# Kernel optimization log

Hardware: AMD Instinct MI355X
Metric: run time of the kernel (lower is better)

The kernel has to match this reference:

```python
import jax, jax.numpy as jnp
import numpy as np

N_HEADS = 8

def gcn_conv(x, edge_index, W, b):
    # PyG GCNConv: add self-loops, symmetric normalization, linear transform + bias
    N = x.shape[0]
    loop = jnp.arange(N)
    src = jnp.concatenate([edge_index[0], loop])
    dst = jnp.concatenate([edge_index[1], loop])
    deg = jax.ops.segment_sum(jnp.ones(src.shape[0], dtype=x.dtype), dst, num_segments=N)
    dinv = jax.lax.rsqrt(jnp.maximum(deg, 1.0))  # deg >= 1 due to self-loops
    norm = dinv[src] * dinv[dst]                 # [E+N]
    h = x @ W                                    # [N, out]
    msg = h[src] * norm[:, None]                 # gather + scale
    return jax.ops.segment_sum(msg, dst, num_segments=N) + b

def layer_norm(x, g, b):
    mu = jnp.mean(x, axis=-1, keepdims=True)
    var = jnp.mean((x - mu) ** 2, axis=-1, keepdims=True)
    return (x - mu) * jax.lax.rsqrt(var + 1e-5) * g + b

def mha(q, kv, Wq, Wk, Wv, Wo):
    B, M, d = q.shape
    dh = d // N_HEADS
    Q = (q @ Wq).reshape(B, M, N_HEADS, dh)
    K = (kv @ Wk).reshape(B, kv.shape[1], N_HEADS, dh)
    V = (kv @ Wv).reshape(B, kv.shape[1], N_HEADS, dh)
    scale = jnp.asarray(1.0 / np.sqrt(dh), q.dtype)
    scores = jnp.einsum('bqhd,bkhd->bhqk', Q, K) * scale
    attn = jax.nn.softmax(scores, axis=-1)
    out = jnp.einsum('bhqk,bkhd->bqhd', attn, V).reshape(B, M, d)
    return out @ Wo

def setup_inputs() -> dict:
    key = jax.random.key(0)
    ks = jax.random.split(key, 24)
    B, M, d, dff, L = 32, 1024, 128, 512, 2
    N, E = B * M, 524288
    s = 0.02
    inp = {
        'enc_out_vari': jax.random.normal(ks[0], (B, M, d), jnp.float32),
        'x_enc': jax.random.normal(ks[1], (B, M, d), jnp.float32),
        'x_raw': jax.random.normal(ks[2], (N, d), jnp.float32),
        'edge_index': jax.random.randint(ks[3], (2, E), 0, N, jnp.int64 if jax.config.jax_enable_x64 else jnp.int32),
        'W_gcn1': s * jax.random.normal(ks[4], (d, d), jnp.float32),
        'b_gcn1': jnp.zeros((d,), jnp.float32),
        'W_gcn2': s * jax.random.normal(ks[5], (d, d), jnp.float32),
        'b_gcn2': jnp.zeros((d,), jnp.float32),
        'Wq': s * jax.random.normal(ks[6], (L, d, d), jnp.float32),
        'Wk': s * jax.random.normal(ks[7], (L, d, d), jnp.float32),
        'Wv': s * jax.random.normal(ks[8], (L, d, d), jnp.float32),
        'Wo': s * jax.random.normal(ks[9], (L, d, d), jnp.float32),
        'Wff1': s * jax.random.normal(ks[10], (L, d, dff), jnp.float32),
        'bff1': jnp.zeros((L, dff), jnp.float32),
        'Wff2': s * jax.random.normal(ks[11], (L, dff, d), jnp.float32),
        'bff2': jnp.zeros((L, d), jnp.float32),
        'ln1_g': jnp.ones((L, d), jnp.float32),
        'ln1_b': jnp.zeros((L, d), jnp.float32),
        'ln2_g': jnp.ones((L, d), jnp.float32),
        'ln2_b': jnp.zeros((L, d), jnp.float32),
    }
    return inp

def reference(enc_out_vari, x_enc, x_raw, edge_index, W_gcn1, b_gcn1, W_gcn2, b_gcn2,
              Wq, Wk, Wv, Wo, Wff1, bff1, Wff2, bff2, ln1_g, ln1_b, ln2_g, ln2_b):
    B, M, d = enc_out_vari.shape
    # GCN stack (dropout is identity in eval mode)
    x1 = jax.nn.relu(gcn_conv(x_raw, edge_index, W_gcn1, b_gcn1))
    x2 = jax.nn.relu(gcn_conv(x1, edge_index, W_gcn2, b_gcn2))
    x = x2.reshape(B, M, d)
    # Transformer encoder: cross-attention from enc_out_vari onto GCN features
    y = enc_out_vari
    L = Wq.shape[0]
    for l in range(L):
        a = mha(y, x, Wq[l], Wk[l], Wv[l], Wo[l])
        y = layer_norm(y + a, ln1_g[l], ln1_b[l])
        f = jax.nn.relu(y @ Wff1[l] + bff1[l]) @ Wff2[l] + bff2[l]
        y = layer_norm(y + f, ln2_g[l], ln2_b[l])
    return y
```

## Files before the change

### kernel.cpp

```cpp
#include <hip/hip_runtime.h>
#include <math.h>


typedef __attribute__((ext_vector_type(8)))  short short8;
typedef __attribute__((ext_vector_type(4)))  float f32x4;
typedef __attribute__((ext_vector_type(16))) float f32x16;

__device__ __forceinline__ unsigned short f2bf(float x) {
    unsigned u = __builtin_bit_cast(unsigned, x);
    u = (u + 0x7FFFu + ((u >> 16) & 1u)) >> 16;
    return (unsigned short)u;
}
__device__ __forceinline__ float bflo(unsigned u) { return __builtin_bit_cast(float, u << 16); }
__device__ __forceinline__ float bfhi(unsigned u) { return __builtin_bit_cast(float, u & 0xffff0000u); }
__device__ __forceinline__ float fast_exp2(float x) {
    float r; asm("v_exp_f32 %0, %1" : "=v"(r) : "v"(x)); return r;
}

__global__ void count_kernel(const int* __restrict__ dst, int* __restrict__ cnt, int E) {
    int e = blockIdx.x * 256 + threadIdx.x;
    if (e < E) atomicAdd(&cnt[dst[e]], 1);
}

__global__ __launch_bounds__(256)
void scanA_kernel(const int* __restrict__ cnt, int* __restrict__ partial)
{
    __shared__ int wsum[4];
    int t = threadIdx.x;
    int v = cnt[blockIdx.x * 256 + t];
    #pragma unroll
    for (int off = 32; off; off >>= 1) v += __shfl_xor(v, off, 64);
    if ((t & 63) == 0) wsum[t >> 6] = v;
    __syncthreads();
    if (t == 0) partial[blockIdx.x] = wsum[0] + wsum[1] + wsum[2] + wsum[3];
}

__global__ __launch_bounds__(128)
void scanB_kernel(const int* __restrict__ partial, int* __restrict__ base)
{
    __shared__ int p[128];
    int t = threadIdx.x;
    int v = partial[t];
    p[t] = v;
    __syncthreads();
    for (int o = 1; o < 128; o <<= 1) {
        int q = (t >= o) ? p[t - o] : 0;
        __syncthreads();
        p[t] += q;
        __syncthreads();
    }
    base[t] = p[t] - v;
}

__global__ __launch_bounds__(256)
void scanC_kernel(const int* __restrict__ cnt, const int* __restrict__ base,
                  int* __restrict__ off, int* __restrict__ cursor,
                  float* __restrict__ dinv, int N, int E)
{
    __shared__ int p[256];
    int t = threadIdx.x, b = blockIdx.x;
    int i = b * 256 + t;
    int c = cnt[i];
    p[t] = c;
    __syncthreads();
    for (int o = 1; o < 256; o <<= 1) {
        int q = (t >= o) ? p[t - o] : 0;
        __syncthreads();
        p[t] += q;
        __syncthreads();
    }
    int ex = base[b] + p[t] - c;
    off[i] = ex;
    cursor[i] = ex;
    dinv[i] = rsqrtf((float)c + 1.0f);
    if (b == 0 && t == 0) off[N] = E;
}

__global__ void place_kernel(const int* __restrict__ src, const int* __restrict__ dst,
                             int* __restrict__ cursor, int* __restrict__ csr_src, int E)
{
    int e = blockIdx.x * 256 + threadIdx.x;
    if (e < E) {
        int p = atomicAdd(&cursor[dst[e]], 1);
        csr_src[p] = src[e];
    }
}

__global__ void conv_kernel(const float* __restrict__ src, unsigned short* __restrict__ dst) {
    int i = blockIdx.x * 256 + threadIdx.x;
    float4 v = ((const float4*)src)[i];
    ushort4 h; h.x = f2bf(v.x); h.y = f2bf(v.y); h.z = f2bf(v.z); h.w = f2bf(v.w);
    ((ushort4*)dst)[i] = h;
}

__global__ void copyconv_kernel(const float* __restrict__ src, float* __restrict__ dstf,
                                unsigned short* __restrict__ dsth) {
    int i = blockIdx.x * 256 + threadIdx.x;
    float4 v = ((const float4*)src)[i];
    ((float4*)dstf)[i] = v;
    ushort4 h; h.x = f2bf(v.x); h.y = f2bf(v.y); h.z = f2bf(v.z); h.w = f2bf(v.w);
    ((ushort4*)dsth)[i] = h;
}

__global__ __launch_bounds__(256)
void wtrans_kernel(const float* Wg1, const float* Wg2, const float* Wq, const float* Wk,
                   const float* Wv, const float* Wo, const float* Wff1, const float* Wff2,
                   unsigned short* __restrict__ out)
{
    const int slot = blockIdx.y;
    const float* src; int ks; int Ns; size_t doff; float scale = 1.0f;
    if      (slot == 0)  { src = Wg1;                        ks = 7; Ns = 128; doff = 0; }
    else if (slot == 1)  { src = Wg2;                        ks = 7; Ns = 128; doff = 16384; }
    else if (slot <= 3)  { src = Wq  + (slot - 2)  * 16384;  ks = 7; Ns = 128; doff = 32768  + (size_t)(slot - 2)  * 16384; scale = 0.36067376022f; }
    else if (slot <= 5)  { src = Wk  + (slot - 4)  * 16384;  ks = 7; Ns = 128; doff = 65536  + (size_t)(slot - 4)  * 32768; }
    else if (slot <= 7)  { src = Wv  + (slot - 6)  * 16384;  ks = 7; Ns = 128; doff = 65536  + (size_t)(slot - 6)  * 32768 + 16384; }
    else if (slot <= 9)  { src = Wo  + (slot - 8)  * 16384;  ks = 7; Ns = 128; doff = 131072 + (size_t)(slot - 8)  * 16384; }
    else if (slot <= 11) { src = Wff1 + (slot - 10) * 65536; ks = 7; Ns = 512; doff = 163840 + (size_t)(slot - 10) * 65536; }
    else                 { src = Wff2 + (slot - 12) * 65536; ks = 9; Ns = 128; doff = 294912 + (size_t)(slot - 12) * 65536; }
    const int total = Ns << ks;
    int id = blockIdx.x * 256 + threadIdx.x;
    if (id >= total) return;
    int n = id >> ks;
    int k = id & ((1 << ks) - 1);
    out[doff + id] = f2bf(src[(size_t)k * Ns + n] * scale);
}

__global__ __launch_bounds__(256)
void gemm64_kernel(const unsigned short* __restrict__ A,
                   const unsigned short* __restrict__ Wt,
                   void* __restrict__ C, void* __restrict__ C2, int K,
                   const float* __restrict__ bias, const float* __restrict__ rowscale,
                   int relu, int mode)
{
    __shared__ unsigned short As[64 * 72];
    __shared__ unsigned short Ws[64 * 72];

    const int tid  = threadIdx.x;
    const int lane = tid & 63, wave = tid >> 6;
    const int m31 = lane & 31, hi = lane >> 5;
    const int row0 = blockIdx.x * 64;
    const int c0   = blockIdx.y * 64;
    const int wrow = (wave & 1) * 32;
    const int wcol = (wave >> 1) * 32;
    const int sr = tid >> 2, sk = (tid & 3) * 16;

    f32x16 acc = {};

    for (int kt = 0; kt < K; kt += 64) {
        if (kt) __syncthreads();
        *(short8*)&As[sr * 72 + sk]     = *(const short8*)&A [(size_t)(row0 + sr) * K + kt + sk];
        *(short8*)&As[sr * 72 + sk + 8] = *(const short8*)&A [(size_t)(row0 + sr) * K + kt + sk + 8];
        *(short8*)&Ws[sr * 72 + sk]     = *(const short8*)&Wt[(size_t)(c0   + sr) * K + kt + sk];
        *(short8*)&Ws[sr * 72 + sk + 8] = *(const short8*)&Wt[(size_t)(c0   + sr) * K + kt + sk + 8];
        __syncthreads();
        #pragma unroll
        for (int ks = 0; ks < 4; ++ks) {
            short8 af = *(const short8*)&As[(wrow + m31) * 72 + ks * 16 + hi * 8];
            short8 bf = *(const short8*)&Ws[(wcol + m31) * 72 + ks * 16 + hi * 8];
            acc = __builtin_amdgcn_mfma_f32_32x32x16_bf16(af, bf, acc, 0, 0, 0);
        }
    }

    const int col = c0 + wcol + m31;
    #pragma unroll
    for (int r = 0; r < 16; ++r) {
        const int row = row0 + wrow + (r & 3) + 8 * (r >> 2) + 4 * hi;
        float v = acc[r];
        if (rowscale) v *= rowscale[row];
        if (bias) v += bias[col];
        if (relu) v = fmaxf(v, 0.0f);
        if (mode == 1) {
            ((unsigned short*)C)[(size_t)row * gridDim.y * 64 + col] = f2bf(v);
        } else {
            if (col < 128) {
                ((unsigned short*)C)[(size_t)row * 128 + col] = f2bf(v);
            } else {
                int ch = col - 128, hh = ch >> 4, dd = ch & 15;
                ((unsigned short*)C2)[(((size_t)(row >> 10) * 8 + hh) * 16 + dd) * 1024
                                      + (row & 1023)] = f2bf(v);
            }
        }
    }
}

__global__ __launch_bounds__(256)
void gemm_ln_kernel(const unsigned short* __restrict__ A,
                    const unsigned short* __restrict__ Wt, int K,
                    const float* __restrict__ bias,
                    const float* __restrict__ resid_in, float* __restrict__ resid_out,
                    unsigned short* __restrict__ yh,
                    const float* __restrict__ lng, const float* __restrict__ lnb)
{
    __shared__ __align__(16) unsigned char smraw[33280];
    unsigned short* As = (unsigned short*)smraw;
    unsigned short* Ws = (unsigned short*)(smraw + 9216);

    const int tid  = threadIdx.x;
    const int lane = tid & 63, wave = tid >> 6;
    const int m31 = lane & 31, hi = lane >> 5;
    const int row0 = blockIdx.x * 64;
    const int wrow = (wave & 1) * 32;
    const int wcol = (wave >> 1) * 64;
    const int sr = tid >> 2, sk = (tid & 3) * 16;
    const int wr = tid >> 1, wo = (tid & 1) * 32;

    f32x16 acc0 = {}, acc1 = {};

    for (int kt = 0; kt < K; kt += 64) {
        if (kt) __syncthreads();
        *(short8*)&As[sr * 72 + sk]      = *(const short8*)&A [(size_t)(row0 + sr) * K + kt + sk];
        *(short8*)&As[sr * 72 + sk + 8]  = *(const short8*)&A [(size_t)(row0 + sr) * K + kt + sk + 8];
        *(short8*)&Ws[wr * 72 + wo]      = *(const short8*)&Wt[(size_t)wr * K + kt + wo];
        *(short8*)&Ws[wr * 72 + wo + 8]  = *(const short8*)&Wt[(size_t)wr * K + kt + wo + 8];
        *(short8*)&Ws[wr * 72 + wo + 16] = *(const short8*)&Wt[(size_t)wr * K + kt + wo + 16];
        *(short8*)&Ws[wr * 72 + wo + 24] = *(const short8*)&Wt[(size_t)wr * K + kt + wo + 24];
        __syncthreads();
        #pragma unroll
        for (int ks = 0; ks < 4; ++ks) {
            short8 af = *(const short8*)&As[(wrow + m31) * 72 + ks * 16 + hi * 8];
            short8 b0 = *(const short8*)&Ws[(wcol + m31) * 72 + ks * 16 + hi * 8];
            short8 b1 = *(const short8*)&Ws[(wcol + 32 + m31) * 72 + ks * 16 + hi * 8];
            acc0 = __builtin_amdgcn_mfma_f32_32x32x16_bf16(af, b0, acc0, 0, 0, 0);
            acc1 = __builtin_amdgcn_mfma_f32_32x32x16_bf16(af, b1, acc1, 0, 0, 0);
        }
    }

    __syncthreads();
    float* Ts = (float*)smraw;
    #pragma unroll
    for (int r = 0; r < 16; ++r) {
        const int rl = wrow + (r & 3) + 8 * (r >> 2) + 4 * hi;
        #pragma unroll
        for (int ct = 0; ct < 2; ++ct) {
            const int col = wcol + ct * 32 + m31;
            float v = ct ? acc1[r] : acc0[r];
            if (bias) v += bias[col];
            Ts[rl * 130 + col] = v;
        }
    }
    __syncthreads();
    const int r  = tid >> 2;
    const int cq = tid & 3;
    const int row = row0 + r;
    float v[32], s1 = 0.f, s2 = 0.f;
    const float* yr = resid_in + (size_t)row * 128 + cq * 32;
    #pragma unroll
    for (int i = 0; i < 8; ++i) {
        float4 yv = *(const float4*)&yr[i * 4];
        float ys[4] = {yv.x, yv.y, yv.z, yv.w};
        #pragma unroll
        for (int j = 0; j < 4; ++j) {
            float t = Ts[r * 130 + cq * 32 + i * 4 + j] + ys[j];
            v[i * 4 + j] = t; s1 += t; s2 += t * t;
        }
    }
    s1 += __shfl_xor(s1, 1, 64); s1 += __shfl_xor(s1, 2, 64);
    s2 += __shfl_xor(s2, 1, 64); s2 += __shfl_xor(s2, 2, 64);
    const float mu  = s1 * (1.0f / 128.0f);
    const float inv = rsqrtf(s2 * (1.0f / 128.0f) - mu * mu + 1e-5f);
    float* outr = resid_out + (size_t)row * 128 + cq * 32;
    unsigned short* yhr = yh + (size_t)row * 128 + cq * 32;
    #pragma unroll
    for (int i = 0; i < 8; ++i) {
        float o0 = (v[i*4+0] - mu) * inv * lng[cq*32 + i*4 + 0] + lnb[cq*32 + i*4 + 0];
        float o1 = (v[i*4+1] - mu) * inv * lng[cq*32 + i*4 + 1] + lnb[cq*32 + i*4 + 1];
        float o2 = (v[i*4+2] - mu) * inv * lng[cq*32 + i*4 + 2] + lnb[cq*32 + i*4 + 2];
        float o3 = (v[i*4+3] - mu) * inv * lng[cq*32 + i*4 + 3] + lnb[cq*32 + i*4 + 3];
        float4 ov; ov.x = o0; ov.y = o1; ov.z = o2; ov.w = o3;
        *(float4*)&outr[i * 4] = ov;
        ushort4 hv; hv.x = f2bf(o0); hv.y = f2bf(o1); hv.z = f2bf(o2); hv.w = f2bf(o3);
        *(ushort4*)&yhr[i * 4] = hv;
    }
}

__global__ __launch_bounds__(256)
void gather_kernel(const unsigned short* __restrict__ hs, const int* __restrict__ csr_off,
                   const int* __restrict__ csr_src, const float* __restrict__ dinv,
                   const float* __restrict__ bias, unsigned short* __restrict__ out, int N)
{
    const int node = blockIdx.x * 4 + (threadIdx.x >> 6);
    const int lane = threadIdx.x & 63;
    const int s0 = csr_off[node], s1 = csr_off[node + 1];
    const unsigned* hsu = (const unsigned*)hs;

    unsigned u = hsu[(size_t)node * 64 + lane];
    float a0 = bflo(u), a1 = bfhi(u);

    for (int base = s0; base < s1; base += 64) {
        int cnt = s1 - base; if (cnt > 64) cnt = 64;
        int idx = (base + lane < s1) ? csr_src[base + lane] : 0;
        int j = 0;
        for (; j + 4 <= cnt; j += 4) {
            size_t sA = (size_t)__shfl(idx, j,     64) * 64;
            size_t sB = (size_t)__shfl(idx, j + 1, 64) * 64;
            size_t sC = (size_t)__shfl(idx, j + 2, 64) * 64;
            size_t sD = (size_t)__shfl(idx, j + 3, 64) * 64;
            unsigned uA = hsu[sA + lane], uB = hsu[sB + lane];
            unsigned uC = hsu[sC + lane], uD = hsu[sD + lane];
            a0 += (bflo(uA) + bflo(uB)) + (bflo(uC) + bflo(uD));
            a1 += (bfhi(uA) + bfhi(uB)) + (bfhi(uC) + bfhi(uD));
        }
        for (; j < cnt; ++j) {
            size_t sb = (size_t)__shfl(idx, j, 64) * 64;
            unsigned ub = hsu[sb + lane];
            a0 += bflo(ub); a1 += bfhi(ub);
        }
    }
    float di = dinv[node];
    float v0 = fmaxf(a0 * di + bias[lane * 2],     0.0f);
    float v1 = fmaxf(a1 * di + bias[lane * 2 + 1], 0.0f);
    ((unsigned*)out)[(size_t)node * 64 + lane] =
        ((unsigned)f2bf(v1) << 16) | (unsigned)f2bf(v0);
}

__global__ __launch_bounds__(256)
void attn_mfma_kernel(const unsigned short* __restrict__ Qh,
                      const unsigned short* __restrict__ Kg,
                      const unsigned short* __restrict__ Vtg,
                      unsigned short* __restrict__ Obh)
{
    __shared__ unsigned short Ks[128 * 40];
    __shared__ unsigned short Vt[16 * 136];
    __shared__ unsigned short Ps[4][16 * 136];

    const int tid  = threadIdx.x;
    const int lane = tid & 63, wave = tid >> 6;
    const int quad = lane >> 4, l16 = lane & 15;
    const int q0 = blockIdx.x * 64, h = blockIdx.y, b = blockIdx.z;

    {
        short8 z = {};
        *(short8*)&Ks[(tid >> 1) * 40 + 16 + (tid & 1) * 8] = z;
    }

    short8 qa = {};
    if (quad < 2) {
        qa = *(const short8*)&Qh[((size_t)b * 1024 + q0 + wave * 16 + l16) * 128 + h * 16 + quad * 8];
    }

    f32x4 o = {0.f, 0.f, 0.f, 0.f};
    float l0[4] = {0.f, 0.f, 0.f, 0.f};
    unsigned short* Pw = &Ps[wave][0];

    for (int k0 = 0; k0 < 1024; k0 += 128) {
        __syncthreads();
        {
            int key = tid >> 1, half = (tid & 1) * 8;
            int slot = (key & 7) * 16 + (key >> 3);
            *(short8*)&Ks[slot * 40 + half] =
                *(const short8*)&Kg[((size_t)b * 1024 + k0 + key) * 128 + h * 16 + half];
            int dim = tid >> 4, kc = (tid & 15) * 8;
            *(short8*)&Vt[dim * 136 + kc] =
                *(const short8*)&Vtg[(((size_t)b * 8 + h) * 16 + dim) * 1024 + k0 + kc];
        }
        __syncthreads();

        f32x4 s[8];
        f32x4 zc = {0.f, 0.f, 0.f, 0.f};
        #pragma unroll
        for (int g = 0; g < 8; ++g) {
            short8 kb = *(const short8*)&Ks[(g * 16 + l16) * 40 + quad * 8];
            s[g] = __builtin_amdgcn_mfma_f32_16x16x32_bf16(qa, kb, zc, 0, 0, 0);
        }

        #pragma unroll
        for (int r = 0; r < 4; ++r) {
            float p0 = fast_exp2(s[0][r]);
            float p1 = fast_exp2(s[1][r]);
            float p2 = fast_exp2(s[2][r]);
            float p3 = fast_exp2(s[3][r]);
            float p4 = fast_exp2(s[4][r]);
            float p5 = fast_exp2(s[5][r]);
            float p6 = fast_exp2(s[6][r]);
            float p7 = fast_exp2(s[7][r]);
            l0[r] += ((p0 + p1) + (p2 + p3)) + ((p4 + p5) + (p6 + p7));
            uint4 pk;
            pk.x = __builtin_amdgcn_perm(__builtin_bit_cast(unsigned, p1),
                                         __builtin_bit_cast(unsigned, p0), 0x07060302u);
            pk.y = __builtin_amdgcn_perm(__builtin_bit_cast(unsigned, p3),
                                         __builtin_bit_cast(unsigned, p2), 0x07060302u);
            pk.z = __builtin_amdgcn_perm(__builtin_bit_cast(unsigned, p5),
                                         __builtin_bit_cast(unsigned, p4), 0x07060302u);
            pk.w = __builtin_amdgcn_perm(__builtin_bit_cast(unsigned, p7),
                                         __builtin_bit_cast(unsigned, p6), 0x07060302u);
            *(uint4*)&Pw[(quad * 4 + r) * 136 + l16 * 8] = pk;
        }
        asm volatile("s_waitcnt lgkmcnt(0)" ::: "memory");
        __builtin_amdgcn_sched_barrier(0);

        #pragma unroll
        for (int t = 0; t < 4; ++t) {
            short8 pa = *(const short8*)&Pw[l16 * 136 + t * 32 + quad * 8];
            short8 vb = *(const short8*)&Vt[l16 * 136 + t * 32 + quad * 8];
            o = __builtin_amdgcn_mfma_f32_16x16x32_bf16(pa, vb, o, 0, 0, 0);
        }
    }

    #pragma unroll
    for (int r = 0; r < 4; ++r) {
        float lr = l0[r];
        #pragma unroll
        for (int off = 1; off < 16; off <<= 1) lr += __shfl_xor(lr, off, 64);
        float linv = 1.0f / lr;
        int qrow = q0 + wave * 16 + quad * 4 + r;
        Obh[((size_t)b * 1024 + qrow) * 128 + h * 16 + l16] = f2bf(o[r] * linv);
    }
}

extern "C" void kernel_launch(void* const* d_in, const int* in_sizes, int n_in,
                              void* d_out, int out_size, void* d_ws, size_t ws_size,
                              hipStream_t stream)
{
    const float* enc  = (const float*)d_in[0];
    const float* xraw = (const float*)d_in[2];
    const int*   ei   = (const int*)d_in[3];
    const float* Wg1  = (const float*)d_in[4];
    const float* bg1  = (const float*)d_in[5];
    const float* Wg2  = (const float*)d_in[6];
    const float* bg2  = (const float*)d_in[7];
    const float* Wq   = (const float*)d_in[8];
    const float* Wk   = (const float*)d_in[9];
    const float* Wv   = (const float*)d_in[10];
    const float* Wo   = (const float*)d_in[11];
    const float* Wff1 = (const float*)d_in[12];
    const float* bff1 = (const float*)d_in[13];
    const float* Wff2 = (const float*)d_in[14];
    const float* bff2 = (const float*)d_in[15];
    const float* ln1g = (const float*)d_in[16];
    const float* ln1b = (const float*)d_in[17];
    const float* ln2g = (const float*)d_in[18];
    const float* ln2b = (const float*)d_in[19];

    const int E  = in_sizes[3] / 2;
    const int N  = in_sizes[2] / 128;
    const int BM = in_sizes[0] / 128;
    const int B  = BM / 1024;
    const int L  = in_sizes[8] / (128 * 128);

    const int* srcE = ei;
    const int* dstE = ei + E;

    const size_t ND = (size_t)N * 128;

    float* ws   = (float*)d_ws;
    float* dinv = ws;
    int* cnt     = (int*)(ws + 32768);
    int* csr_off = cnt + N;
    int* cursor  = csr_off + N + 4;
    int* csr_src = cursor + N;
    int* partial = csr_src + E;
    int* pbase   = partial + 128;
    float* bufY  = (float*)(pbase + 128);
    unsigned short* ush   = (unsigned short*)(bufY + ND);
    unsigned short* bufYh = ush;
    unsigned short* bufBh = bufYh + ND;
    unsigned short* region = bufBh + ND;
    unsigned short* Qh  = region;
    unsigned short* Kg  = region + ND;
    unsigned short* Vtg = region + 2 * ND;
    unsigned short* Th  = region + 3 * ND;
    unsigned short* Hh  = region;
    unsigned short* hsh   = region;
    unsigned short* xrawh = region + ND;
    unsigned short* wt  = region + 4 * ND;

    hipMemsetAsync(cnt, 0, (size_t)N * sizeof(int), stream);
    count_kernel<<<(E + 255) / 256, 256, 0, stream>>>(dstE, cnt, E);
    scanA_kernel<<<N / 256, 256, 0, stream>>>(cnt, partial);
    scanB_kernel<<<1, 128, 0, stream>>>(partial, pbase);
    scanC_kernel<<<N / 256, 256, 0, stream>>>(cnt, pbase, csr_off, cursor, dinv, N, E);
    place_kernel<<<(E + 255) / 256, 256, 0, stream>>>(srcE, dstE, cursor, csr_src, E);

    conv_kernel<<<(int)(ND / 1024), 256, 0, stream>>>(xraw, xrawh);
    copyconv_kernel<<<(int)(ND / 1024), 256, 0, stream>>>(enc, bufY, bufYh);
    wtrans_kernel<<<dim3(256, 14), 256, 0, stream>>>(Wg1, Wg2, Wq, Wk, Wv, Wo, Wff1, Wff2, wt);

    gemm64_kernel<<<dim3(N / 64, 2), 256, 0, stream>>>(xrawh, wt, hsh, nullptr, 128,
        nullptr, dinv, 0, 1);
    gather_kernel<<<N / 4, 256, 0, stream>>>(hsh, csr_off, csr_src, dinv, bg1, bufBh, N);
    gemm64_kernel<<<dim3(N / 64, 2), 256, 0, stream>>>(bufBh, wt + 16384, hsh, nullptr, 128,
        nullptr, dinv, 0, 1);
    gather_kernel<<<N / 4, 256, 0, stream>>>(hsh, csr_off, csr_src, dinv, bg2, bufBh, N);

    for (int l = 0; l < L; ++l) {
        const unsigned short* wtq  = wt + 32768  + (size_t)l * 16384;
        const unsigned short* wtkv = wt + 65536  + (size_t)l * 32768;
        const unsigned short* wto  = wt + 131072 + (size_t)l * 16384;
        const unsigned short* wtf1 = wt + 163840 + (size_t)l * 65536;
        const unsigned short* wtf2 = wt + 294912 + (size_t)l * 65536;

        gemm64_kernel<<<dim3(BM / 64, 2), 256, 0, stream>>>(bufYh, wtq, Qh, nullptr, 128,
            nullptr, nullptr, 0, 1);
        gemm64_kernel<<<dim3(N / 64, 4), 256, 0, stream>>>(bufBh, wtkv, Kg, Vtg, 128,
            nullptr, nullptr, 0, 2);

        attn_mfma_kernel<<<dim3(16, 8, B), 256, 0, stream>>>(Qh, Kg, Vtg, Th);

        gemm_ln_kernel<<<BM / 64, 256, 0, stream>>>(Th, wto, 128, nullptr,
            bufY, bufY, bufYh, ln1g + l * 128, ln1b + l * 128);

        gemm64_kernel<<<dim3(BM / 64, 8), 256, 0, stream>>>(bufYh, wtf1, Hh, nullptr, 128,
            bff1 + l * 512, nullptr, 1, 1);

        float* rout = (l == L - 1) ? (float*)d_out : bufY;
        gemm_ln_kernel<<<BM / 64, 256, 0, stream>>>(Hh, wtf2, 512, bff2 + l * 128,
            bufY, rout, bufYh, ln2g + l * 128, ln2b + l * 128);
    }
}
```

Before: 572.7 us.

## Prefetch next K/V tile into registers and pre-permute V in GEMM epilogue

The attention kernel now loads the next 128-key K and V tile into registers while the current tile is being computed, so global loads overlap with MFMA and softmax work. This replaces the old pattern of sync, load, sync at the top of each iteration. The K shared-memory tile loses its zero padding and slot permutation; to keep keys matched, the projection GEMM epilogue now writes transposed V in a permuted key order. This adds register pressure and couples the GEMM output layout to the attention kernel's internal ordering.

Result: no change. 570.0 us (-0.5%).

```diff
diff --git a/kernel.cpp b/kernel.cpp
--- a/kernel.cpp
+++ b/kernel.cpp
@@ -176,8 +176,11 @@
                 ((unsigned short*)C)[(size_t)row * 128 + col] = f2bf(v);
             } else {
                 int ch = col - 128, hh = ch >> 4, dd = ch & 15;
+                int kg = row & 1023;
+                int w  = kg & 127;
+                int kpos = (kg & ~127) | ((w & 15) * 8) | (w >> 4);
                 ((unsigned short*)C2)[(((size_t)(row >> 10) * 8 + hh) * 16 + dd) * 1024
-                                      + (row & 1023)] = f2bf(v);
+                                      + kpos] = f2bf(v);
             }
         }
     }
@@ -319,19 +322,19 @@
                       const unsigned short* __restrict__ Vtg,
                       unsigned short* __restrict__ Obh)
 {
-    __shared__ unsigned short Ks[128 * 40];
-    __shared__ unsigned short Vt[16 * 136];
-    __shared__ unsigned short Ps[4][16 * 136];
+    __shared__ __align__(16) unsigned short Ks[128 * 16];
+    __shared__ __align__(16) unsigned short Vt[16 * 136];
+    __shared__ __align__(16) unsigned short Ps[4][16 * 136];
 
     const int tid  = threadIdx.x;
     const int lane = tid & 63, wave = tid >> 6;
     const int quad = lane >> 4, l16 = lane & 15;
     const int q0 = blockIdx.x * 64, h = blockIdx.y, b = blockIdx.z;
 
-    {
-        short8 z = {};
-        *(short8*)&Ks[(tid >> 1) * 40 + 16 + (tid & 1) * 8] = z;
-    }
+    const int key  = tid >> 1, half = (tid & 1) * 8;
+    const int dim  = tid >> 4, kc = (tid & 15) * 8;
+    const unsigned short* Kp = &Kg[((size_t)b * 1024 + key) * 128 + h * 16 + half];
+    const unsigned short* Vp = &Vtg[(((size_t)b * 8 + h) * 16 + dim) * 1024 + kc];
 
     short8 qa = {};
     if (quad < 2) {
@@ -341,17 +344,17 @@
     f32x4 o = {0.f, 0.f, 0.f, 0.f};
     float l0[4] = {0.f, 0.f, 0.f, 0.f};
     unsigned short* Pw = &Ps[wave][0];
-
-    for (int k0 = 0; k0 < 1024; k0 += 128) {
-        __syncthreads();
-        {
-            int key = tid >> 1, half = (tid & 1) * 8;
-            int slot = (key & 7) * 16 + (key >> 3);
-            *(short8*)&Ks[slot * 40 + half] =
-                *(const short8*)&Kg[((size_t)b * 1024 + k0 + key) * 128 + h * 16 + half];
-            int dim = tid >> 4, kc = (tid & 15) * 8;
-            *(short8*)&Vt[dim * 136 + kc] =
-                *(const short8*)&Vtg[(((size_t)b * 8 + h) * 16 + dim) * 1024 + k0 + kc];
+    const int kread = (quad & 1) * 8;
+
+    short8 kreg = *(const short8*)(Kp);
+    short8 vreg = *(const short8*)(Vp);
+
+    for (int it = 0; it < 8; ++it) {
+        *(short8*)&Ks[key * 16 + half] = kreg;
+        *(short8*)&Vt[dim * 136 + kc]  = vreg;
+        if (it < 7) {
+            kreg = *(const short8*)(Kp + (size_t)(it + 1) * 128 * 128);
+            vreg = *(const short8*)(Vp + (it + 1) * 128);
         }
         __syncthreads();
 
@@ -359,7 +362,7 @@
         f32x4 zc = {0.f, 0.f, 0.f, 0.f};
         #pragma unroll
         for (int g = 0; g < 8; ++g) {
-            short8 kb = *(const short8*)&Ks[(g * 16 + l16) * 40 + quad * 8];
+            short8 kb = *(const short8*)&Ks[(g * 16 + l16) * 16 + kread];
             s[g] = __builtin_amdgcn_mfma_f32_16x16x32_bf16(qa, kb, zc, 0, 0, 0);
         }
 
@@ -394,6 +397,7 @@
             short8 vb = *(const short8*)&Vt[l16 * 136 + t * 32 + quad * 8];
             o = __builtin_amdgcn_mfma_f32_16x16x32_bf16(pa, vb, o, 0, 0, 0);
         }
+        if (it < 7) __syncthreads();
     }
 
     #pragma unroll
```
